# Performance work log

Hardware: AMD Instinct MI355X
Metric: run time of the kernel (lower is better)

Reference implementation:

```python
import jax, jax.numpy as jnp
import numpy as np

VOCAB = 100000
EMBED = 128

def setup_inputs() -> dict:
    key = jax.random.key(0)
    k1, k2, k3 = jax.random.split(key, 3)
    x = jax.random.randint(k1, (4096, 200), 0, VOCAB, dtype=jnp.int64)
    # torch Linear(vocab, embed): weight [embed, vocab], bias [embed]
    W = jax.random.normal(k2, (EMBED, VOCAB), dtype=jnp.float32) * (1.0 / np.sqrt(VOCAB))
    b = jax.random.normal(k3, (EMBED,), dtype=jnp.float32) * 0.01
    return {"x": x, "W": W, "b": b}

def reference(x, W, b):
    # one_hot(x) @ W.T + b  ==  gather rows of W.T at x, then add bias.
    # Same math as the original scatter+Linear, expressed as a row-gather.
    y = jnp.take(W.T, x, axis=0)  # [B, T, EMBED]
    return y + b
```

## Files before the change

kernel.cpp:

```cpp
#include <hip/hip_runtime.h>


#define EMB 128

typedef float fx4 __attribute__((ext_vector_type(4)));

__global__ void transpose_bias_kernel(const float* __restrict__ W,
                                      const float* __restrict__ bias,
                                      float* __restrict__ Wt, int V) {
    __shared__ float lds[64 * 129];
    const int v0 = blockIdx.x * 64;
    const int t  = threadIdx.x;

    #pragma unroll 8
    for (int j = t; j < 128 * 64; j += 256) {
        const int e    = j >> 6;
        const int vloc = j & 63;
        const int v    = v0 + vloc;
        float val = 0.0f;
        if (v < V) val = __builtin_nontemporal_load(&W[(size_t)e * V + v]);
        lds[vloc * 129 + e] = val;
    }
    __syncthreads();

    #pragma unroll 8
    for (int j = t; j < 64 * 128; j += 256) {
        const int vloc = j >> 7;
        const int e    = j & 127;
        const int v    = v0 + vloc;
        if (v < V) Wt[(size_t)v * EMB + e] = lds[vloc * 129 + e] + bias[e];
    }
}

__global__ __launch_bounds__(256) void gather_rows_deep(
        const int* __restrict__ idx, const float* __restrict__ Wt,
        float* __restrict__ out, int ntok) {
    const int t = threadIdx.x;
    const int q = t & 31;
    const int g = t >> 5;
    const int niter  = (ntok + 127) >> 7;
    const int stride = gridDim.x;

    int it = blockIdx.x;
    if (it >= niter) return;

    int rows[16];
    {
        const int tok0 = it << 7;
        #pragma unroll
        for (int p = 0; p < 16; ++p) {
            const int tok = tok0 + g + (p << 3);
            rows[p] = (tok < ntok) ? idx[tok] : 0;
        }
    }

    while (it < niter) {
        const int it_n = it + stride;

        int rows_n[16];
        if (it_n < niter) {
            const int tok0n = it_n << 7;
            #pragma unroll
            for (int p = 0; p < 16; ++p) {
                const int tok = tok0n + g + (p << 3);
                rows_n[p] = (tok < ntok) ? idx[tok] : 0;
            }
        } else {
            #pragma unroll
            for (int p = 0; p < 16; ++p) rows_n[p] = 0;
        }

        fx4 v[16];
        #pragma unroll
        for (int p = 0; p < 16; ++p)
            v[p] = ((const fx4*)(Wt + ((size_t)rows[p] << 7)))[q];

        const int tok0 = it << 7;
        #pragma unroll
        for (int p = 0; p < 16; ++p) {
            const int tok = tok0 + g + (p << 3);
            if (tok < ntok)
                __builtin_nontemporal_store(
                    v[p], (fx4*)(out + ((size_t)tok << 7)) + q);
        }

        #pragma unroll
        for (int p = 0; p < 16; ++p) rows[p] = rows_n[p];
        it = it_n;
    }
}

__global__ void gather_direct_kernel(const int* __restrict__ idx,
                                     const float* __restrict__ W,
                                     const float* __restrict__ bias,
                                     float* __restrict__ out, int ntok, int V) {
    const long long total  = (long long)ntok * EMB;
    const long long stride = (long long)gridDim.x * blockDim.x;
    for (long long i = (long long)blockIdx.x * blockDim.x + threadIdx.x;
         i < total; i += stride) {
        const int token = (int)(i >> 7);
        const int e     = (int)(i & (EMB - 1));
        out[i] = W[(size_t)e * V + idx[token]] + bias[e];
    }
}

extern "C" void kernel_launch(void* const* d_in, const int* in_sizes, int n_in,
                              void* d_out, int out_size, void* d_ws, size_t ws_size,
                              hipStream_t stream) {
    const int*   x = (const int*)d_in[0];
    const float* W = (const float*)d_in[1];
    const float* b = (const float*)d_in[2];
    float* out = (float*)d_out;

    const int ntok = in_sizes[0];
    const int V    = in_sizes[1] / EMB;

    const size_t need = (size_t)V * EMB * sizeof(float);
    if (ws_size >= need) {
        float* Wt = (float*)d_ws;
        const int tblocks = (V + 63) / 64;
        transpose_bias_kernel<<<tblocks, 256, 0, stream>>>(W, b, Wt, V);
        gather_rows_deep<<<1280, 256, 0, stream>>>(x, Wt, out, ntok);
    } else {
        gather_direct_kernel<<<2048, 256, 0, stream>>>(x, W, b, out, ntok, V);
    }
}
```

Measured before the change: 518.1 us.

## Bucket tokens by vocabulary chunk before gathering transposed embedding rows

```diff
diff --git a/kernel.cpp b/kernel.cpp
--- a/kernel.cpp
+++ b/kernel.cpp
@@ -2,15 +2,20 @@
 
 
 #define EMB 128
+#define CH_LOG 11
+#define MAXCHUNK 64
 
 typedef float fx4 __attribute__((ext_vector_type(4)));
 
 __global__ void transpose_bias_kernel(const float* __restrict__ W,
                                       const float* __restrict__ bias,
-                                      float* __restrict__ Wt, int V) {
+                                      float* __restrict__ Wt,
+                                      int* __restrict__ counts, int V) {
     __shared__ float lds[64 * 129];
     const int v0 = blockIdx.x * 64;
     const int t  = threadIdx.x;
+
+    if (blockIdx.x == 0 && t < MAXCHUNK) counts[t] = 0;
 
     #pragma unroll 8
     for (int j = t; j < 128 * 64; j += 256) {
@@ -32,6 +37,93 @@
     }
 }
 
+__global__ __launch_bounds__(256) void hist_kernel(const int* __restrict__ idx,
+                                                   int ntok,
+                                                   int* __restrict__ counts) {
+    __shared__ int lc[MAXCHUNK];
+    const int t = threadIdx.x;
+    if (t < MAXCHUNK) lc[t] = 0;
+    __syncthreads();
+
+    const int stride = gridDim.x * blockDim.x;
+    for (int i = blockIdx.x * blockDim.x + t; i < ntok; i += stride)
+        atomicAdd(&lc[idx[i] >> CH_LOG], 1);
+
+    __syncthreads();
+    if (t < MAXCHUNK && lc[t]) atomicAdd(&counts[t], lc[t]);
+}
+
+__global__ void prefix_kernel(int* __restrict__ counts,
+                              int* __restrict__ base) {
+    if (threadIdx.x == 0 && blockIdx.x == 0) {
+        int run = 0;
+        for (int c = 0; c < MAXCHUNK; ++c) {
+            base[c] = run;
+            run += counts[c];
+            counts[c] = base[c];
+        }
+        base[MAXCHUNK] = run;
+    }
+}
+
+__global__ __launch_bounds__(256) void scatter_kernel(const int* __restrict__ idx,
+                                                      int ntok,
+                                                      int* __restrict__ gcur,
+                                                      int2* __restrict__ rec) {
+    __shared__ int lc[MAXCHUNK];
+    __shared__ int lb[MAXCHUNK];
+    const int t = threadIdx.x;
+    if (t < MAXCHUNK) lc[t] = 0;
+    __syncthreads();
+
+    const int j0 = blockIdx.x * 512 + t;
+    int row0 = 0, row1 = 0, c0 = -1, c1 = -1, s0 = 0, s1 = 0;
+    if (j0 < ntok)       { row0 = idx[j0];       c0 = row0 >> CH_LOG; }
+    if (j0 + 256 < ntok) { row1 = idx[j0 + 256]; c1 = row1 >> CH_LOG; }
+    if (c0 >= 0) s0 = atomicAdd(&lc[c0], 1);
+    if (c1 >= 0) s1 = atomicAdd(&lc[c1], 1);
+    __syncthreads();
+
+    if (t < MAXCHUNK) lb[t] = lc[t] ? atomicAdd(&gcur[t], lc[t]) : 0;
+    __syncthreads();
+
+    if (c0 >= 0) rec[lb[c0] + s0] = make_int2(j0, row0);
+    if (c1 >= 0) rec[lb[c1] + s1] = make_int2(j0 + 256, row1);
+}
+
+__global__ __launch_bounds__(256) void gather_bucketed(
+        const int2* __restrict__ rec, const int* __restrict__ base,
+        const float* __restrict__ Wt, float* __restrict__ out) {
+    const int t  = threadIdx.x;
+    const int q  = t & 31;
+    const int g  = t >> 5;
+    const int x  = blockIdx.x & 7;
+    const int bi = blockIdx.x >> 3;
+    const int nb = gridDim.x >> 3;
+
+    for (int c = x; c < MAXCHUNK; c += 8) {
+        const int s = base[c];
+        const int n = base[c + 1] - s;
+        for (int i0 = bi * 64; i0 < n; i0 += nb * 64) {
+            int2 r[8];
+            #pragma unroll
+            for (int p = 0; p < 8; ++p) {
+                const int i = i0 + g + (p << 3);
+                r[p] = (i < n) ? rec[s + i] : make_int2(-1, 0);
+            }
+            fx4 v[8];
+            #pragma unroll
+            for (int p = 0; p < 8; ++p)
+                v[p] = ((const fx4*)(Wt + ((size_t)r[p].y << 7)))[q];
+            #pragma unroll
+            for (int p = 0; p < 8; ++p)
+                if (r[p].x >= 0)
+                    __builtin_nontemporal_store(
+                        v[p], (fx4*)(out + ((size_t)r[p].x << 7)) + q);
+        }
+    }
+}
+
 __global__ __launch_bounds__(256) void gather_rows_deep(
         const int* __restrict__ idx, const float* __restrict__ Wt,
         float* __restrict__ out, int ntok) {
@@ -41,41 +133,18 @@
     const int niter  = (ntok + 127) >> 7;
     const int stride = gridDim.x;
 
-    int it = blockIdx.x;
-    if (it >= niter) return;
-
-    int rows[16];
-    {
+    for (int it = blockIdx.x; it < niter; it += stride) {
         const int tok0 = it << 7;
+        int rows[16];
         #pragma unroll
         for (int p = 0; p < 16; ++p) {
             const int tok = tok0 + g + (p << 3);
             rows[p] = (tok < ntok) ? idx[tok] : 0;
         }
-    }
-
-    while (it < niter) {
-        const int it_n = it + stride;
-
-        int rows_n[16];
-        if (it_n < niter) {
-            const int tok0n = it_n << 7;
-            #pragma unroll
-            for (int p = 0; p < 16; ++p) {
-                const int tok = tok0n + g + (p << 3);
-                rows_n[p] = (tok < ntok) ? idx[tok] : 0;
-            }
-        } else {
-            #pragma unroll
-            for (int p = 0; p < 16; ++p) rows_n[p] = 0;
-        }
-
         fx4 v[16];
         #pragma unroll
         for (int p = 0; p < 16; ++p)
             v[p] = ((const fx4*)(Wt + ((size_t)rows[p] << 7)))[q];
-
-        const int tok0 = it << 7;
         #pragma unroll
         for (int p = 0; p < 16; ++p) {
             const int tok = tok0 + g + (p << 3);
@@ -83,10 +152,6 @@
                 __builtin_nontemporal_store(
                     v[p], (fx4*)(out + ((size_t)tok << 7)) + q);
         }
-
-        #pragma unroll
-        for (int p = 0; p < 16; ++p) rows[p] = rows_n[p];
-        it = it_n;
     }
 }
 
@@ -115,11 +180,28 @@
     const int ntok = in_sizes[0];
     const int V    = in_sizes[1] / EMB;
 
-    const size_t need = (size_t)V * EMB * sizeof(float);
-    if (ws_size >= need) {
+    const size_t wt_bytes = (size_t)V * EMB * sizeof(float);
+    const size_t offA = (wt_bytes + 511) & ~(size_t)511;
+    const size_t offB = offA + 512;
+    const size_t offC = offB + 512;
+    const size_t need_bucketed = offC + (size_t)ntok * sizeof(int2);
+
+    if (ws_size >= need_bucketed && V <= (MAXCHUNK << CH_LOG)) {
+        float* Wt   = (float*)d_ws;
+        int*   cur  = (int*)((char*)d_ws + offA);
+        int*   base = (int*)((char*)d_ws + offB);
+        int2*  rec  = (int2*)((char*)d_ws + offC);
+
+        const int tblocks = (V + 63) / 64;
+        transpose_bias_kernel<<<tblocks, 256, 0, stream>>>(W, b, Wt, cur, V);
+        hist_kernel<<<1280, 256, 0, stream>>>(x, ntok, cur);
+        prefix_kernel<<<1, 64, 0, stream>>>(cur, base);
+        scatter_kernel<<<(ntok + 511) / 512, 256, 0, stream>>>(x, ntok, cur, rec);
+        gather_bucketed<<<1280, 256, 0, stream>>>(rec, base, Wt, out);
+    } else if (ws_size >= wt_bytes) {
         float* Wt = (float*)d_ws;
         const int tblocks = (V + 63) / 64;
-        transpose_bias_kernel<<<tblocks, 256, 0, stream>>>(W, b, Wt, V);
+        transpose_bias_kernel<<<tblocks, 256, 0, stream>>>(W, b, Wt, (int*)nullptr, V);
         gather_rows_deep<<<1280, 256, 0, stream>>>(x, Wt, out, ntok);
     } else {
         gather_direct_kernel<<<2048, 256, 0, stream>>>(x, W, b, out, ntok, V);
```

Measured after the change: 548.3 us. 5.8% more time.
